# Kernel optimization log

Measured on AMD Instinct MI355X. Metric: run time of the kernel, lower is better.

## Reference

```python
import jax, jax.numpy as jnp
import numpy as np

N_ATOMS = 25000
N_PAIRS = 500000
N_PROP = 16
C = 64          # channel width of pp/pi/ii/out layers
N_BASIS = 4     # radial basis functions per pair
DEPTH = 4       # number of GC blocks


def setup_inputs() -> dict:
    key = jax.random.key(0)
    ks = jax.random.split(key, 16)

    def w(k, shape):
        fan_in = shape[-2]
        return jax.random.normal(k, shape, jnp.float32) / jnp.sqrt(jnp.float32(fan_in))

    return {
        "ind_2": jax.random.randint(ks[0], (N_PAIRS, 2), 0, N_ATOMS),
        "prop": jax.random.normal(ks[1], (N_ATOMS, N_PROP), jnp.float32),
        "basis": jax.random.uniform(ks[2], (N_PAIRS, N_BASIS), jnp.float32),
        "pp0_w1": w(ks[3], (N_PROP, C)),
        "pp0_b1": jnp.zeros((C,), jnp.float32),
        "pp_w1": w(ks[4], (DEPTH - 1, C, C)),
        "pp_b1": jnp.zeros((DEPTH - 1, C), jnp.float32),
        "pp_w2": w(ks[5], (DEPTH, C, C)),
        "pp_b2": jnp.zeros((DEPTH, C), jnp.float32),
        "pi_w1": w(ks[6], (DEPTH, 2 * C, C)),
        "pi_b1": jnp.zeros((DEPTH, C), jnp.float32),
        "pi_w2": w(ks[7], (DEPTH, C, C * N_BASIS)),
        "pi_b2": jnp.zeros((DEPTH, C * N_BASIS), jnp.float32),
        "ii_w1": w(ks[8], (DEPTH, C, C)),
        "ii_w2": w(ks[9], (DEPTH, C, C)),
        "res0_w": w(ks[10], (N_PROP, C)),
        "out_w1": w(ks[11], (DEPTH, C, C)),
        "out_b1": jnp.zeros((DEPTH, C), jnp.float32),
        "out_w2": w(ks[12], (DEPTH, C, C)),
        "out_b2": jnp.zeros((DEPTH, C), jnp.float32),
        "out_wo": w(ks[13], (DEPTH, C, 1)),
    }


def _pinet_forward(ind_2, prop, basis,
                   pp0_w1, pp0_b1, pp_w1, pp_b1, pp_w2, pp_b2,
                   pi_w1, pi_b1, pi_w2, pi_b2,
                   ii_w1, ii_w2, res0_w,
                   out_w1, out_b1, out_w2, out_b2, out_wo):
    act = jnp.tanh
    n_atoms = prop.shape[0]
    n_basis = basis.shape[-1]
    c = pi_w2.shape[-1] // n_basis  # pi output channels
    depth = pp_w2.shape[0]
    ind_i = ind_2[:, 0]
    ind_j = ind_2[:, 1]

    p = prop
    output = jnp.zeros((n_atoms, out_wo.shape[-1]), p.dtype)
    for d in range(depth):
        # PPLayer (FFLayer with bias)
        if d == 0:
            h = act(p @ pp0_w1 + pp0_b1)
        else:
            h = act(p @ pp_w1[d - 1] + pp_b1[d - 1])
        h = act(h @ pp_w2[d] + pp_b2[d])
        # PILayer: gather pair endpoints, concat, FFLayer, basis contraction
        pij = jnp.concatenate([h[ind_i], h[ind_j]], axis=-1)  # (P, 2C)
        ww = act(pij @ pi_w1[d] + pi_b1[d])                   # (P, C)
        ww = act(ww @ pi_w2[d] + pi_b2[d])                    # (P, C*B)
        ww = ww.reshape(-1, c, n_basis)                       # (P, C, B)
        inter = jnp.einsum('pcb,pb->pc', ww, basis)           # (P, C)
        # IILayer (FFLayer, no bias)
        inter = act(inter @ ii_w1[d])
        inter = act(inter @ ii_w2[d])
        # IPLayer: scatter-sum pairs back to atoms
        newp = jax.ops.segment_sum(inter, ind_i, num_segments=n_atoms)
        # ResUpdate: linear projection if dims differ (block 0), else plain sum
        p = (p @ res0_w + newp) if d == 0 else (p + newp)
        # OutLayer: FFLayer + biasless linear, accumulated over depth
        o = act(p @ out_w1[d] + out_b1[d])
        o = act(o @ out_w2[d] + out_b2[d])
        output = output + o @ out_wo[d]
    return output


def reference(ind_2, prop, basis,
              pp0_w1, pp0_b1, pp_w1, pp_b1, pp_w2, pp_b2,
              pi_w1, pi_b1, pi_w2, pi_b2,
              ii_w1, ii_w2, res0_w,
              out_w1, out_b1, out_w2, out_b2, out_wo):
    return _pinet_forward(ind_2, prop, basis,
                          pp0_w1, pp0_b1, pp_w1, pp_b1, pp_w2, pp_b2,
                          pi_w1, pi_b1, pi_w2, pi_b2,
                          ii_w1, ii_w2, res0_w,
                          out_w1, out_b1, out_w2, out_b2, out_wo)
```

## Files before the change

kernel.cpp:

```cpp
#include <hip/hip_runtime.h>
#include <hip/hip_bf16.h>

#define N_ATOMS 25000
#define N_PAIRS 500000
#define DEPTH 4

typedef _Float16 f16x8 __attribute__((ext_vector_type(8)));
typedef float f32x16 __attribute__((ext_vector_type(16)));
typedef unsigned short u16;

__device__ __forceinline__ float tanh_fast(float x) {
    float e = __expf(2.0f * x);
    return 1.0f - 2.0f * __builtin_amdgcn_rcpf(e + 1.0f);
}

__device__ __forceinline__ void split_h(float x, u16& hi, u16& lo) {
    _Float16 h = (_Float16)x;
    _Float16 l = (_Float16)(x - (float)h);
    hi = *(u16*)&h;
    lo = *(u16*)&l;
}

__device__ __forceinline__ void bar_lgkm() {
    asm volatile("s_waitcnt lgkmcnt(0)" ::: "memory");
    __builtin_amdgcn_s_barrier();
}

__device__ __forceinline__ int swz8(int u) { return u ^ ((u >> 5) & 7); }

__global__ __launch_bounds__(256)
void prep_kernel(const float* __restrict__ piW1, const float* __restrict__ piW2,
                 const float* __restrict__ iiW1, const float* __restrict__ iiW2,
                 u16* __restrict__ img1, u16* __restrict__ img2, u16* __restrict__ imgab) {
    int gid = blockIdx.x * 256 + threadIdx.x;
    int d = gid >> 15, e = gid & 32767;
    u16 hi, lo;
    if (e < 8192) {
        int k = e >> 6, n = e & 63;
        split_h(piW1[d * 8192 + e], hi, lo);
        int ntw = n >> 5, colb = n & 31;
        int ks = k >> 4, lh = (k >> 3) & 1, j = k & 7;
        int off = ((ntw * 8 + ks) * 64 + lh * 32 + colb) * 8 + j;
        img1[d * 16384 + 0 * 8192 + off] = hi;
        img1[d * 16384 + 1 * 8192 + off] = lo;
    } else if (e < 24576) {
        int s = e - 8192;
        int k = s >> 8, n = s & 255;
        split_h(piW2[d * 16384 + s], hi, lo);
        int ch = n >> 2, t = n & 3;
        int ntw = ch >> 5, colb = ch & 31;
        int ks = k >> 4, lh = (k >> 3) & 1, j = k & 7;
        int off = (((ntw * 4 + t) * 4 + ks) * 64 + lh * 32 + colb) * 8 + j;
        img2[d * 32768 + 0 * 16384 + off] = hi;
        img2[d * 32768 + 1 * 16384 + off] = lo;
    } else {
        int stage = (e < 28672) ? 0 : 1;
        int s = e - (stage ? 28672 : 24576);
        int k = s >> 6, n = s & 63;
        float x = stage ? iiW2[d * 4096 + s] : iiW1[d * 4096 + s];
        split_h(x, hi, lo);
        int ntw = n >> 5, colb = n & 31;
        int ks = k >> 4, lh = (k >> 3) & 1, j = k & 7;
        int off = ((ntw * 4 + ks) * 64 + lh * 32 + colb) * 8 + j;
        imgab[d * 16384 + (stage * 2 + 0) * 4096 + off] = hi;
        imgab[d * 16384 + (stage * 2 + 1) * 4096 + off] = lo;
    }
}

__global__ __launch_bounds__(256)
void prep_b2(const float* __restrict__ piB2, float* __restrict__ b2p) {
    int d = blockIdx.x, n = threadIdx.x;
    int ch = n >> 2, t = n & 3;
    int np = (ch >> 5) * 128 + t * 32 + (ch & 31);
    b2p[d * 256 + np] = piB2[d * 256 + n];
}

template <int K, bool IS_D0>
__global__ __launch_bounds__(256)
void atom_mlp(const float* __restrict__ p_in,
              const float* __restrict__ W1, const float* __restrict__ b1,
              const float* __restrict__ W2, const float* __restrict__ b2,
              const float* __restrict__ res0_w,
              _Float16* __restrict__ h_hi, _Float16* __restrict__ h_lo,
              float* __restrict__ acc_out) {
    __shared__ float sP[4][64];
    __shared__ float sH[4][64];
    int tid = threadIdx.x;
    int al = tid >> 6, c = tid & 63;
    int a = blockIdx.x * 4 + al;
    if (c < K) sP[al][c] = p_in[a * K + c];
    __syncthreads();
    float s = b1[c];
#pragma unroll
    for (int k = 0; k < K; ++k) s += sP[al][k] * W1[k * 64 + c];
    float t1 = tanh_fast(s);
    float r;
    if (IS_D0) {
        r = 0.f;
#pragma unroll
        for (int k = 0; k < 16; ++k) r += sP[al][k] * res0_w[k * 64 + c];
    } else {
        r = sP[al][c];
    }
    acc_out[a * 64 + c] = r;
    sH[al][c] = t1;
    __syncthreads();
    float s2 = b2[c];
#pragma unroll
    for (int k = 0; k < 64; ++k) s2 += sH[al][k] * W2[k * 64 + c];
    float hv = tanh_fast(s2);
    _Float16 hb = (_Float16)hv;
    h_hi[a * 64 + c] = hb;
    h_lo[a * 64 + c] = (_Float16)(hv - (float)hb);
}

__global__ __launch_bounds__(256)
void out_kernel(const float* __restrict__ p,
                const float* __restrict__ W1, const float* __restrict__ b1,
                const float* __restrict__ W2, const float* __restrict__ b2,
                const float* __restrict__ wo,
                float* __restrict__ out, int store) {
    __shared__ float sP[4][64];
    __shared__ float sH[4][64];
    int tid = threadIdx.x;
    int al = tid >> 6, c = tid & 63;
    int a = blockIdx.x * 4 + al;
    sP[al][c] = p[a * 64 + c];
    __syncthreads();
    float s = b1[c];
#pragma unroll
    for (int k = 0; k < 64; ++k) s += sP[al][k] * W1[k * 64 + c];
    sH[al][c] = tanh_fast(s);
    __syncthreads();
    float s2 = b2[c];
#pragma unroll
    for (int k = 0; k < 64; ++k) s2 += sH[al][k] * W2[k * 64 + c];
    float v = tanh_fast(s2) * wo[c];
#pragma unroll
    for (int off = 32; off > 0; off >>= 1) v += __shfl_down(v, off, 64);
    if (c == 0) {
        if (store) out[a] = v;
        else out[a] += v;
    }
}

__global__ __launch_bounds__(256)
void fused_out_atom(const float* __restrict__ p,
                    const float* __restrict__ oW1, const float* __restrict__ ob1,
                    const float* __restrict__ oW2, const float* __restrict__ ob2,
                    const float* __restrict__ wo,
                    const float* __restrict__ aW1, const float* __restrict__ ab1,
                    const float* __restrict__ aW2, const float* __restrict__ ab2,
                    float* __restrict__ out, int store,
                    _Float16* __restrict__ h_hi, _Float16* __restrict__ h_lo,
                    float* __restrict__ acc_out) {
    __shared__ float sP[4][64];
    __shared__ float sHo[4][64];
    __shared__ float sHa[4][64];
    int tid = threadIdx.x;
    int al = tid >> 6, c = tid & 63;
    int a = blockIdx.x * 4 + al;
    float pv = p[a * 64 + c];
    sP[al][c] = pv;
    acc_out[a * 64 + c] = pv;
    __syncthreads();
    float so = ob1[c], sa = ab1[c];
#pragma unroll
    for (int k = 0; k < 64; ++k) {
        float x = sP[al][k];
        so += x * oW1[k * 64 + c];
        sa += x * aW1[k * 64 + c];
    }
    sHo[al][c] = tanh_fast(so);
    sHa[al][c] = tanh_fast(sa);
    __syncthreads();
    float s2o = ob2[c], s2a = ab2[c];
#pragma unroll
    for (int k = 0; k < 64; ++k) {
        s2o += sHo[al][k] * oW2[k * 64 + c];
        s2a += sHa[al][k] * aW2[k * 64 + c];
    }
    float v = tanh_fast(s2o) * wo[c];
#pragma unroll
    for (int off = 32; off > 0; off >>= 1) v += __shfl_down(v, off, 64);
    if (c == 0) {
        if (store) out[a] = v;
        else out[a] += v;
    }
    float hv = tanh_fast(s2a);
    _Float16 hb = (_Float16)hv;
    h_hi[a * 64 + c] = hb;
    h_lo[a * 64 + c] = (_Float16)(hv - (float)hb);
}

#define MFMA __builtin_amdgcn_mfma_f32_32x32x16_f16

__global__ __launch_bounds__(512, 2)
void pair_kernel(const _Float16* __restrict__ hhi,
                 const _Float16* __restrict__ hlo,
                 const int* __restrict__ ind2,
                 const float* __restrict__ basis,
                 const u16* __restrict__ img1,
                 const u16* __restrict__ img2,
                 const u16* __restrict__ imgab,
                 const float* __restrict__ piB1,
                 const float* __restrict__ b2p,
                 float* __restrict__ accp) {
    __shared__ __attribute__((aligned(16))) _Float16 sW2[32768];
    __shared__ __attribute__((aligned(16))) _Float16 sW1lo[8192];
    __shared__ __attribute__((aligned(16))) _Float16 sA[16384];
    __shared__ __attribute__((aligned(16))) _Float16 sAlo[8192];
    __shared__ __attribute__((aligned(16))) _Float16 sPing[8192];
    __shared__ float sBas[2][128 * 4];
    __shared__ int sIdx[2][128];

    const int tid = threadIdx.x;
    for (int i = tid; i < 4096; i += 512) ((uint4*)sW2)[i] = ((const uint4*)img2)[i];
    for (int i = tid; i < 1024; i += 512) ((uint4*)sW1lo)[i] = ((const uint4*)(img1 + 8192))[i];

    const int l = tid & 63;
    const int w = tid >> 6;
    const int mt = w >> 1, ntw = w & 1;
    const int col = l & 31, kg = l >> 5;
    const int ch = ntw * 32 + col;
    const int chks = ch >> 4, chlh = (ch >> 3) & 1, chj = ch & 7;

    int rb[4], wb[4];
    {
        const int wxor = 2 * chks + chlh;
#pragma unroll
        for (int c = 0; c < 4; ++c) {
            rb[c] = (l ^ (kg + 2 * c)) << 4;
            wb[c] = (mt * 4 + chks) * 1024 + chlh * 512 + ((((c) + 4 * kg) ^ wxor) << 4) + chj * 2;
        }
    }
    const int mtsA = mt << 13;
    const int mts  = mt << 12;

    f16x8 w1h[8], fa[2][4], fb[2][4];
#pragma unroll
    for (int ks = 0; ks < 8; ++ks)
        w1h[ks] = *(const f16x8*)(img1 + ntw * 4096 + ks * 512 + l * 8);
#pragma unroll
    for (int hl = 0; hl < 2; ++hl)
#pragma unroll
        for (int ks = 0; ks < 4; ++ks) {
            fa[hl][ks] = *(const f16x8*)(imgab + (0 * 2 + hl) * 4096 + ntw * 2048 + ks * 512 + l * 8);
            fb[hl][ks] = *(const f16x8*)(imgab + (1 * 2 + hl) * 4096 + ntw * 2048 + ks * 512 + l * 8);
        }
    const float b1v = piB1[ch];
    float b2v[4];
#pragma unroll
    for (int t = 0; t < 4; ++t) b2v[t] = b2p[ntw * 128 + t * 32 + col];

    const int nTiles = (N_PAIRS + 127) >> 7;

    auto gather = [&](int tile, int pb) {
        int base = tile << 7;
        if (tid < 128) {
            int p = base + tid;
            float4 bv = (p < N_PAIRS) ? ((const float4*)basis)[p] : make_float4(0.f, 0.f, 0.f, 0.f);
            *(float4*)&sBas[pb][tid * 4] = bv;
            sIdx[pb][tid] = (p < N_PAIRS) ? ind2[2 * p] : 0;
        }
#pragma unroll
        for (int it = 0; it < 6; ++it) {
            int id = it * 512 + tid;
            if (id < 2048) {
                int m = id >> 4, half = (id >> 3) & 1, seg = id & 7;
                int p = base + m;
                uint4 v = make_uint4(0u, 0u, 0u, 0u);
                if (p < N_PAIRS) {
                    int row = ind2[2 * p + half];
                    v = *(const uint4*)(hhi + row * 64 + seg * 8);
                }
                int mtd = m >> 5, lrow = m & 31;
                int ks = half * 4 + (seg >> 1), lh = seg & 1;
                int u = (mtd * 8 + ks) * 64 + lh * 32 + lrow;
                *(uint4*)(sA + swz8(u) * 8) = v;
            } else {
                int e = id - 2048;
                int m = e >> 3, seg = e & 7;
                int p = base + m;
                uint4 v = make_uint4(0u, 0u, 0u, 0u);
                if (p < N_PAIRS) {
                    int row = ind2[2 * p];
                    v = *(const uint4*)(hlo + row * 64 + seg * 8);
                }
                int mtd = m >> 5, lrow = m & 31;
                int ks = seg >> 1, lh = seg & 1;
                int u = (mtd * 4 + ks) * 64 + lh * 32 + lrow;
                *(uint4*)(sAlo + swz8(u) * 8) = v;
            }
        }
    };
    gather(blockIdx.x, 0);
    __syncthreads();

    int pb = 0;
    for (int tile = blockIdx.x; tile < nTiles; tile += gridDim.x) {
        const int base = tile << 7;

        {
            f32x16 acc = {};
            const char* blo = (const char*)(sW1lo + ntw * 4096 + l * 8);
#pragma unroll
            for (int ks = 0; ks < 8; ++ks) {
                f16x8 a = *(const f16x8*)((const char*)sA + mtsA + ks * 1024 + rb[ks & 3]);
                acc = MFMA(a, w1h[ks], acc, 0, 0, 0);
                acc = MFMA(a, *(const f16x8*)(blo + ks * 1024), acc, 0, 0, 0);
            }
#pragma unroll
            for (int ks = 0; ks < 4; ++ks) {
                f16x8 a = *(const f16x8*)((const char*)sAlo + mts + ks * 1024 + rb[ks]);
                acc = MFMA(a, w1h[ks], acc, 0, 0, 0);
            }
#pragma unroll
            for (int r = 0; r < 16; ++r)
                *(u16*)((char*)sPing + wb[r & 3] + ((r >> 2) << 7)) =
                    __builtin_bit_cast(u16, (_Float16)tanh_fast(acc[r] + b1v));
        }
        bar_lgkm();

        {
            f32x16 acc[4] = {{}, {}, {}, {}};
#pragma unroll
            for (int ks = 0; ks < 4; ++ks) {
                f16x8 a = *(const f16x8*)((const char*)sPing + mts + ks * 1024 + rb[ks]);
#pragma unroll
                for (int t = 0; t < 4; ++t) {
                    acc[t] = MFMA(a, *(const f16x8*)(sW2 + ((ntw * 4 + t) * 4 + ks) * 512 + l * 8), acc[t], 0, 0, 0);
                    acc[t] = MFMA(a, *(const f16x8*)(sW2 + 16384 + ((ntw * 4 + t) * 4 + ks) * 512 + l * 8), acc[t], 0, 0, 0);
                }
            }
#pragma unroll
            for (int r = 0; r < 16; ++r) {
                int lrow = (r & 3) + 8 * (r >> 2) + 4 * kg;
                int row = mt * 32 + lrow;
                float4 bas = *(const float4*)&sBas[pb][row * 4];
                float s = tanh_fast(acc[0][r] + b2v[0]) * bas.x
                        + tanh_fast(acc[1][r] + b2v[1]) * bas.y
                        + tanh_fast(acc[2][r] + b2v[2]) * bas.z
                        + tanh_fast(acc[3][r] + b2v[3]) * bas.w;
                *(u16*)((char*)sA + wb[r & 3] + ((r >> 2) << 7)) =
                    __builtin_bit_cast(u16, (_Float16)s);
            }
        }
        bar_lgkm();

        {
            f32x16 acc = {};
#pragma unroll
            for (int ks = 0; ks < 4; ++ks) {
                f16x8 a = *(const f16x8*)((const char*)sA + mts + ks * 1024 + rb[ks]);
                acc = MFMA(a, fa[0][ks], acc, 0, 0, 0);
                acc = MFMA(a, fa[1][ks], acc, 0, 0, 0);
            }
#pragma unroll
            for (int r = 0; r < 16; ++r)
                *(u16*)((char*)sPing + wb[r & 3] + ((r >> 2) << 7)) =
                    __builtin_bit_cast(u16, (_Float16)tanh_fast(acc[r]));
        }
        bar_lgkm();

        {
            f16x8 afr[4];
#pragma unroll
            for (int ks = 0; ks < 4; ++ks)
                afr[ks] = *(const f16x8*)((const char*)sPing + mts + ks * 1024 + rb[ks]);

            gather(tile + gridDim.x, pb ^ 1);

            f32x16 acc = {};
#pragma unroll
            for (int ks = 0; ks < 4; ++ks) {
                acc = MFMA(afr[ks], fb[0][ks], acc, 0, 0, 0);
                acc = MFMA(afr[ks], fb[1][ks], acc, 0, 0, 0);
            }
#pragma unroll
            for (int r = 0; r < 16; ++r) {
                int lrow = (r & 3) + 8 * (r >> 2) + 4 * kg;
                int p = base + mt * 32 + lrow;
                if (p < N_PAIRS)
                    atomicAdd(&accp[sIdx[pb][mt * 32 + lrow] * 64 + ch], tanh_fast(acc[r]));
            }
        }
        bar_lgkm();
        pb ^= 1;
    }
}

extern "C" void kernel_launch(void* const* d_in, const int* in_sizes, int n_in,
                              void* d_out, int out_size, void* d_ws, size_t ws_size,
                              hipStream_t stream) {
    const int* ind2 = (const int*)d_in[0];
    const float* prop = (const float*)d_in[1];
    const float* basis = (const float*)d_in[2];
    const float* pp0_w1 = (const float*)d_in[3];
    const float* pp0_b1 = (const float*)d_in[4];
    const float* pp_w1 = (const float*)d_in[5];
    const float* pp_b1 = (const float*)d_in[6];
    const float* pp_w2 = (const float*)d_in[7];
    const float* pp_b2 = (const float*)d_in[8];
    const float* pi_w1 = (const float*)d_in[9];
    const float* pi_b1 = (const float*)d_in[10];
    const float* pi_w2 = (const float*)d_in[11];
    const float* pi_b2 = (const float*)d_in[12];
    const float* ii_w1 = (const float*)d_in[13];
    const float* ii_w2 = (const float*)d_in[14];
    const float* res0_w = (const float*)d_in[15];
    const float* out_w1 = (const float*)d_in[16];
    const float* out_b1 = (const float*)d_in[17];
    const float* out_w2 = (const float*)d_in[18];
    const float* out_b2 = (const float*)d_in[19];
    const float* out_wo = (const float*)d_in[20];
    float* out = (float*)d_out;

    float* B0 = (float*)d_ws;
    float* B1 = B0 + N_ATOMS * 64;
    _Float16* Hhi = (_Float16*)(B1 + N_ATOMS * 64);
    _Float16* Hlo = Hhi + N_ATOMS * 64;
    u16* img1 = (u16*)(Hlo + N_ATOMS * 64);
    u16* img2 = img1 + 4 * 16384;
    u16* imgab = img2 + 4 * 32768;
    float* b2p = (float*)(imgab + 4 * 16384);
    float* pbuf[2] = {B0, B1};

    prep_kernel<<<512, 256, 0, stream>>>(pi_w1, pi_w2, ii_w1, ii_w2, img1, img2, imgab);
    prep_b2<<<4, 256, 0, stream>>>(pi_b2, b2p);

    for (int d = 0; d < DEPTH; ++d) {
        float* acc = pbuf[d & 1];
        if (d == 0) {
            atom_mlp<16, true><<<N_ATOMS / 4, 256, 0, stream>>>(
                prop, pp0_w1, pp0_b1, pp_w2, pp_b2, res0_w, Hhi, Hlo, acc);
        } else {
            const float* pin = pbuf[(d - 1) & 1];
            fused_out_atom<<<N_ATOMS / 4, 256, 0, stream>>>(
                pin,
                out_w1 + (d - 1) * 4096, out_b1 + (d - 1) * 64,
                out_w2 + (d - 1) * 4096, out_b2 + (d - 1) * 64, out_wo + (d - 1) * 64,
                pp_w1 + (d - 1) * 4096, pp_b1 + (d - 1) * 64,
                pp_w2 + d * 4096, pp_b2 + d * 64,
                out, (d - 1) == 0 ? 1 : 0,
                Hhi, Hlo, acc);
        }
        pair_kernel<<<256, 512, 0, stream>>>(
            Hhi, Hlo, ind2, basis,
            img1 + d * 16384, img2 + d * 32768, imgab + d * 16384,
            pi_b1 + d * 64, b2p + d * 256, acc);
    }
    out_kernel<<<N_ATOMS / 4, 256, 0, stream>>>(
        pbuf[(DEPTH - 1) & 1], out_w1 + (DEPTH - 1) * 4096, out_b1 + (DEPTH - 1) * 64,
        out_w2 + (DEPTH - 1) * 4096, out_b2 + (DEPTH - 1) * 64, out_wo + (DEPTH - 1) * 64,
        out, 0);
}
```

Before: 1.043 ms.

## Precompute per-atom pi first-layer projections and gather them in the pair kernel

The first pi layer is linear in the concatenated pair features, so it is split into per-atom projections U = h·W1[:64] and V = h·W1[64:], computed once per atom in the atom MLP kernels. The pair kernel then gathers fp32 U/V rows, adds them with the bias and applies tanh, which removes the per-pair W1 MFMA stage and the hi/lo fp16 split of h. The pair kernel also moves to 192-pair tiles with 768 threads, reads the ii weights from LDS instead of registers, and processes the basis contraction in two passes to save registers. In exchange it gathers twice as many bytes per pair (fp32 instead of fp16), drops the double-buffered gather of the next tile, and adds atom-side matmul work.

```diff
diff --git a/kernel.cpp b/kernel.cpp
--- a/kernel.cpp
+++ b/kernel.cpp
@@ -4,6 +4,8 @@
 #define N_ATOMS 25000
 #define N_PAIRS 500000
 #define DEPTH 4
+#define TILE 192
+#define PTHREADS 768
 
 typedef _Float16 f16x8 __attribute__((ext_vector_type(8)));
 typedef float f32x16 __attribute__((ext_vector_type(16)));
@@ -19,11 +21,6 @@
     _Float16 l = (_Float16)(x - (float)h);
     hi = *(u16*)&h;
     lo = *(u16*)&l;
-}
-
-__device__ __forceinline__ void bar_lgkm() {
-    asm volatile("s_waitcnt lgkmcnt(0)" ::: "memory");
-    __builtin_amdgcn_s_barrier();
 }
 
 __device__ __forceinline__ int swz8(int u) { return u ^ ((u >> 5) & 7); }
@@ -81,10 +78,12 @@
               const float* __restrict__ W1, const float* __restrict__ b1,
               const float* __restrict__ W2, const float* __restrict__ b2,
               const float* __restrict__ res0_w,
-              _Float16* __restrict__ h_hi, _Float16* __restrict__ h_lo,
+              const float* __restrict__ piW1d,
+              float* __restrict__ Uo, float* __restrict__ Vo,
               float* __restrict__ acc_out) {
     __shared__ float sP[4][64];
     __shared__ float sH[4][64];
+    __shared__ float sH2[4][64];
     int tid = threadIdx.x;
     int al = tid >> 6, c = tid & 63;
     int a = blockIdx.x * 4 + al;
@@ -109,9 +108,17 @@
 #pragma unroll
     for (int k = 0; k < 64; ++k) s2 += sH[al][k] * W2[k * 64 + c];
     float hv = tanh_fast(s2);
-    _Float16 hb = (_Float16)hv;
-    h_hi[a * 64 + c] = hb;
-    h_lo[a * 64 + c] = (_Float16)(hv - (float)hb);
+    sH2[al][c] = hv;
+    __syncthreads();
+    float su = 0.f, sv = 0.f;
+#pragma unroll
+    for (int k = 0; k < 64; ++k) {
+        float x = sH2[al][k];
+        su += x * piW1d[k * 64 + c];
+        sv += x * piW1d[(64 + k) * 64 + c];
+    }
+    Uo[a * 64 + c] = su;
+    Vo[a * 64 + c] = sv;
 }
 
 __global__ __launch_bounds__(256)
@@ -152,7 +159,8 @@
                     const float* __restrict__ aW1, const float* __restrict__ ab1,
                     const float* __restrict__ aW2, const float* __restrict__ ab2,
                     float* __restrict__ out, int store,
-                    _Float16* __restrict__ h_hi, _Float16* __restrict__ h_lo,
+                    const float* __restrict__ piW1d,
+                    float* __restrict__ Uo, float* __restrict__ Vo,
                     float* __restrict__ acc_out) {
     __shared__ float sP[4][64];
     __shared__ float sHo[4][64];
@@ -188,35 +196,41 @@
         else out[a] += v;
     }
     float hv = tanh_fast(s2a);
-    _Float16 hb = (_Float16)hv;
-    h_hi[a * 64 + c] = hb;
-    h_lo[a * 64 + c] = (_Float16)(hv - (float)hb);
+    sP[al][c] = hv;
+    __syncthreads();
+    float su = 0.f, sv = 0.f;
+#pragma unroll
+    for (int k = 0; k < 64; ++k) {
+        float x = sP[al][k];
+        su += x * piW1d[k * 64 + c];
+        sv += x * piW1d[(64 + k) * 64 + c];
+    }
+    Uo[a * 64 + c] = su;
+    Vo[a * 64 + c] = sv;
 }
 
 #define MFMA __builtin_amdgcn_mfma_f32_32x32x16_f16
 
-__global__ __launch_bounds__(512, 2)
-void pair_kernel(const _Float16* __restrict__ hhi,
-                 const _Float16* __restrict__ hlo,
+__global__ __launch_bounds__(PTHREADS, 3)
+void pair_kernel(const float* __restrict__ Uin,
+                 const float* __restrict__ Vin,
                  const int* __restrict__ ind2,
                  const float* __restrict__ basis,
-                 const u16* __restrict__ img1,
                  const u16* __restrict__ img2,
                  const u16* __restrict__ imgab,
                  const float* __restrict__ piB1,
                  const float* __restrict__ b2p,
                  float* __restrict__ accp) {
     __shared__ __attribute__((aligned(16))) _Float16 sW2[32768];
-    __shared__ __attribute__((aligned(16))) _Float16 sW1lo[8192];
-    __shared__ __attribute__((aligned(16))) _Float16 sA[16384];
-    __shared__ __attribute__((aligned(16))) _Float16 sAlo[8192];
-    __shared__ __attribute__((aligned(16))) _Float16 sPing[8192];
-    __shared__ float sBas[2][128 * 4];
-    __shared__ int sIdx[2][128];
+    __shared__ __attribute__((aligned(16))) u16 sAB[16384];
+    __shared__ __attribute__((aligned(16))) _Float16 bufA[12288];
+    __shared__ __attribute__((aligned(16))) _Float16 bufB[12288];
+    __shared__ float sBas[TILE * 4];
+    __shared__ int sIdx[TILE];
 
     const int tid = threadIdx.x;
-    for (int i = tid; i < 4096; i += 512) ((uint4*)sW2)[i] = ((const uint4*)img2)[i];
-    for (int i = tid; i < 1024; i += 512) ((uint4*)sW1lo)[i] = ((const uint4*)(img1 + 8192))[i];
+    for (int i = tid; i < 4096; i += PTHREADS) ((uint4*)sW2)[i] = ((const uint4*)img2)[i];
+    for (int i = tid; i < 2048; i += PTHREADS) ((uint4*)sAB)[i] = ((const uint4*)imgab)[i];
 
     const int l = tid & 63;
     const int w = tid >> 6;
@@ -234,159 +248,134 @@
             wb[c] = (mt * 4 + chks) * 1024 + chlh * 512 + ((((c) + 4 * kg) ^ wxor) << 4) + chj * 2;
         }
     }
-    const int mtsA = mt << 13;
-    const int mts  = mt << 12;
-
-    f16x8 w1h[8], fa[2][4], fb[2][4];
-#pragma unroll
-    for (int ks = 0; ks < 8; ++ks)
-        w1h[ks] = *(const f16x8*)(img1 + ntw * 4096 + ks * 512 + l * 8);
-#pragma unroll
-    for (int hl = 0; hl < 2; ++hl)
-#pragma unroll
-        for (int ks = 0; ks < 4; ++ks) {
-            fa[hl][ks] = *(const f16x8*)(imgab + (0 * 2 + hl) * 4096 + ntw * 2048 + ks * 512 + l * 8);
-            fb[hl][ks] = *(const f16x8*)(imgab + (1 * 2 + hl) * 4096 + ntw * 2048 + ks * 512 + l * 8);
-        }
-    const float b1v = piB1[ch];
+    const int mts = mt << 12;
+
+    const int m = tid >> 2, ksel = tid & 3;
+    const int mtd = m >> 5, lrow = m & 31;
+    const int u0 = (mtd * 4 + ksel) * 64 + lrow;
+    const int wA0 = swz8(u0) * 16, wA1 = swz8(u0 + 32) * 16;
+
+    float b1p[16];
+#pragma unroll
+    for (int z = 0; z < 16; ++z) b1p[z] = piB1[ksel * 16 + z];
     float b2v[4];
 #pragma unroll
     for (int t = 0; t < 4; ++t) b2v[t] = b2p[ntw * 128 + t * 32 + col];
 
-    const int nTiles = (N_PAIRS + 127) >> 7;
-
-    auto gather = [&](int tile, int pb) {
-        int base = tile << 7;
-        if (tid < 128) {
+    const int nTiles = (N_PAIRS + TILE - 1) / TILE;
+
+    float ur[16], vr[16];
+    auto loadUV = [&](int tile) {
+        int p = tile * TILE + m;
+        bool ok = (tile < nTiles) && (p < N_PAIRS);
+        int2 ij = ok ? ((const int2*)ind2)[p] : make_int2(0, 0);
+        const float* up = Uin + ij.x * 64 + ksel * 16;
+        const float* vp = Vin + ij.y * 64 + ksel * 16;
+        float4 z4 = make_float4(0.f, 0.f, 0.f, 0.f);
+#pragma unroll
+        for (int q = 0; q < 4; ++q) {
+            float4 a = ok ? *(const float4*)(up + q * 4) : z4;
+            float4 b = ok ? *(const float4*)(vp + q * 4) : z4;
+            ur[q * 4 + 0] = a.x; ur[q * 4 + 1] = a.y; ur[q * 4 + 2] = a.z; ur[q * 4 + 3] = a.w;
+            vr[q * 4 + 0] = b.x; vr[q * 4 + 1] = b.y; vr[q * 4 + 2] = b.z; vr[q * 4 + 3] = b.w;
+        }
+    };
+    loadUV(blockIdx.x);
+
+    for (int tile = blockIdx.x; tile < nTiles; tile += gridDim.x) {
+        const int base = tile * TILE;
+
+        if (tid < TILE) {
             int p = base + tid;
             float4 bv = (p < N_PAIRS) ? ((const float4*)basis)[p] : make_float4(0.f, 0.f, 0.f, 0.f);
-            *(float4*)&sBas[pb][tid * 4] = bv;
-            sIdx[pb][tid] = (p < N_PAIRS) ? ind2[2 * p] : 0;
-        }
-#pragma unroll
-        for (int it = 0; it < 6; ++it) {
-            int id = it * 512 + tid;
-            if (id < 2048) {
-                int m = id >> 4, half = (id >> 3) & 1, seg = id & 7;
-                int p = base + m;
-                uint4 v = make_uint4(0u, 0u, 0u, 0u);
-                if (p < N_PAIRS) {
-                    int row = ind2[2 * p + half];
-                    v = *(const uint4*)(hhi + row * 64 + seg * 8);
+            *(float4*)&sBas[tid * 4] = bv;
+            sIdx[tid] = (p < N_PAIRS) ? ind2[2 * p] : 0;
+        }
+        {
+            f16x8 lo8, hi8;
+#pragma unroll
+            for (int z = 0; z < 8; ++z)
+                lo8[z] = (_Float16)tanh_fast(ur[z] + vr[z] + b1p[z]);
+#pragma unroll
+            for (int z = 0; z < 8; ++z)
+                hi8[z] = (_Float16)tanh_fast(ur[8 + z] + vr[8 + z] + b1p[8 + z]);
+            *(f16x8*)((char*)bufA + wA0) = lo8;
+            *(f16x8*)((char*)bufA + wA1) = hi8;
+        }
+        __syncthreads();
+
+        {
+            f16x8 afr[4];
+#pragma unroll
+            for (int ks = 0; ks < 4; ++ks)
+                afr[ks] = *(const f16x8*)((const char*)bufA + mts + ks * 1024 + rb[ks]);
+            float s[16];
+#pragma unroll
+            for (int r = 0; r < 16; ++r) s[r] = 0.f;
+#pragma unroll
+            for (int pp = 0; pp < 2; ++pp) {
+                f32x16 a0 = {}, a1 = {};
+                const int t0 = 2 * pp, t1 = 2 * pp + 1;
+#pragma unroll
+                for (int ks = 0; ks < 4; ++ks) {
+                    a0 = MFMA(afr[ks], *(const f16x8*)(sW2 + ((ntw * 4 + t0) * 4 + ks) * 512 + l * 8), a0, 0, 0, 0);
+                    a0 = MFMA(afr[ks], *(const f16x8*)(sW2 + 16384 + ((ntw * 4 + t0) * 4 + ks) * 512 + l * 8), a0, 0, 0, 0);
+                    a1 = MFMA(afr[ks], *(const f16x8*)(sW2 + ((ntw * 4 + t1) * 4 + ks) * 512 + l * 8), a1, 0, 0, 0);
+                    a1 = MFMA(afr[ks], *(const f16x8*)(sW2 + 16384 + ((ntw * 4 + t1) * 4 + ks) * 512 + l * 8), a1, 0, 0, 0);
                 }
-                int mtd = m >> 5, lrow = m & 31;
-                int ks = half * 4 + (seg >> 1), lh = seg & 1;
-                int u = (mtd * 8 + ks) * 64 + lh * 32 + lrow;
-                *(uint4*)(sA + swz8(u) * 8) = v;
-            } else {
-                int e = id - 2048;
-                int m = e >> 3, seg = e & 7;
-                int p = base + m;
-                uint4 v = make_uint4(0u, 0u, 0u, 0u);
-                if (p < N_PAIRS) {
-                    int row = ind2[2 * p];
-                    v = *(const uint4*)(hlo + row * 64 + seg * 8);
-                }
-                int mtd = m >> 5, lrow = m & 31;
-                int ks = seg >> 1, lh = seg & 1;
-                int u = (mtd * 4 + ks) * 64 + lh * 32 + lrow;
-                *(uint4*)(sAlo + swz8(u) * 8) = v;
-            }
-        }
-    };
-    gather(blockIdx.x, 0);
-    __syncthreads();
-
-    int pb = 0;
-    for (int tile = blockIdx.x; tile < nTiles; tile += gridDim.x) {
-        const int base = tile << 7;
-
-        {
-            f32x16 acc = {};
-            const char* blo = (const char*)(sW1lo + ntw * 4096 + l * 8);
-#pragma unroll
-            for (int ks = 0; ks < 8; ++ks) {
-                f16x8 a = *(const f16x8*)((const char*)sA + mtsA + ks * 1024 + rb[ks & 3]);
-                acc = MFMA(a, w1h[ks], acc, 0, 0, 0);
-                acc = MFMA(a, *(const f16x8*)(blo + ks * 1024), acc, 0, 0, 0);
-            }
-#pragma unroll
-            for (int ks = 0; ks < 4; ++ks) {
-                f16x8 a = *(const f16x8*)((const char*)sAlo + mts + ks * 1024 + rb[ks]);
-                acc = MFMA(a, w1h[ks], acc, 0, 0, 0);
-            }
-#pragma unroll
-            for (int r = 0; r < 16; ++r)
-                *(u16*)((char*)sPing + wb[r & 3] + ((r >> 2) << 7)) =
-                    __builtin_bit_cast(u16, (_Float16)tanh_fast(acc[r] + b1v));
-        }
-        bar_lgkm();
-
-        {
-            f32x16 acc[4] = {{}, {}, {}, {}};
-#pragma unroll
-            for (int ks = 0; ks < 4; ++ks) {
-                f16x8 a = *(const f16x8*)((const char*)sPing + mts + ks * 1024 + rb[ks]);
-#pragma unroll
-                for (int t = 0; t < 4; ++t) {
-                    acc[t] = MFMA(a, *(const f16x8*)(sW2 + ((ntw * 4 + t) * 4 + ks) * 512 + l * 8), acc[t], 0, 0, 0);
-                    acc[t] = MFMA(a, *(const f16x8*)(sW2 + 16384 + ((ntw * 4 + t) * 4 + ks) * 512 + l * 8), acc[t], 0, 0, 0);
+#pragma unroll
+                for (int r = 0; r < 16; ++r) {
+                    int lr2 = (r & 3) + 8 * (r >> 2) + 4 * kg;
+                    int row = mt * 32 + lr2;
+                    float2 bb = *(const float2*)&sBas[row * 4 + 2 * pp];
+                    s[r] += tanh_fast(a0[r] + b2v[t0]) * bb.x + tanh_fast(a1[r] + b2v[t1]) * bb.y;
                 }
             }
 #pragma unroll
-            for (int r = 0; r < 16; ++r) {
-                int lrow = (r & 3) + 8 * (r >> 2) + 4 * kg;
-                int row = mt * 32 + lrow;
-                float4 bas = *(const float4*)&sBas[pb][row * 4];
-                float s = tanh_fast(acc[0][r] + b2v[0]) * bas.x
-                        + tanh_fast(acc[1][r] + b2v[1]) * bas.y
-                        + tanh_fast(acc[2][r] + b2v[2]) * bas.z
-                        + tanh_fast(acc[3][r] + b2v[3]) * bas.w;
-                *(u16*)((char*)sA + wb[r & 3] + ((r >> 2) << 7)) =
-                    __builtin_bit_cast(u16, (_Float16)s);
+            for (int r = 0; r < 16; ++r)
+                *(u16*)((char*)bufB + wb[r & 3] + ((r >> 2) << 7)) =
+                    __builtin_bit_cast(u16, (_Float16)s[r]);
+        }
+        __syncthreads();
+
+        {
+            f32x16 ah = {}, al2 = {};
+#pragma unroll
+            for (int ks = 0; ks < 4; ++ks) {
+                f16x8 a = *(const f16x8*)((const char*)bufB + mts + ks * 1024 + rb[ks]);
+                ah  = MFMA(a, *(const f16x8*)(sAB + 0 * 4096 + ntw * 2048 + ks * 512 + l * 8), ah, 0, 0, 0);
+                al2 = MFMA(a, *(const f16x8*)(sAB + 1 * 4096 + ntw * 2048 + ks * 512 + l * 8), al2, 0, 0, 0);
             }
-        }
-        bar_lgkm();
-
-        {
-            f32x16 acc = {};
-#pragma unroll
-            for (int ks = 0; ks < 4; ++ks) {
-                f16x8 a = *(const f16x8*)((const char*)sA + mts + ks * 1024 + rb[ks]);
-                acc = MFMA(a, fa[0][ks], acc, 0, 0, 0);
-                acc = MFMA(a, fa[1][ks], acc, 0, 0, 0);
-            }
 #pragma unroll
             for (int r = 0; r < 16; ++r)
-                *(u16*)((char*)sPing + wb[r & 3] + ((r >> 2) << 7)) =
-                    __builtin_bit_cast(u16, (_Float16)tanh_fast(acc[r]));
-        }
-        bar_lgkm();
+                *(u16*)((char*)bufA + wb[r & 3] + ((r >> 2) << 7)) =
+                    __builtin_bit_cast(u16, (_Float16)tanh_fast(ah[r] + al2[r]));
+        }
+        __syncthreads();
 
         {
             f16x8 afr[4];
 #pragma unroll
             for (int ks = 0; ks < 4; ++ks)
-                afr[ks] = *(const f16x8*)((const char*)sPing + mts + ks * 1024 + rb[ks]);
-
-            gather(tile + gridDim.x, pb ^ 1);
-
-            f32x16 acc = {};
+                afr[ks] = *(const f16x8*)((const char*)bufA + mts + ks * 1024 + rb[ks]);
+
+            loadUV(tile + gridDim.x);
+
+            f32x16 ah = {}, al2 = {};
 #pragma unroll
             for (int ks = 0; ks < 4; ++ks) {
-                acc = MFMA(afr[ks], fb[0][ks], acc, 0, 0, 0);
-                acc = MFMA(afr[ks], fb[1][ks], acc, 0, 0, 0);
+                ah  = MFMA(afr[ks], *(const f16x8*)(sAB + 2 * 4096 + ntw * 2048 + ks * 512 + l * 8), ah, 0, 0, 0);
+                al2 = MFMA(afr[ks], *(const f16x8*)(sAB + 3 * 4096 + ntw * 2048 + ks * 512 + l * 8), al2, 0, 0, 0);
             }
 #pragma unroll
             for (int r = 0; r < 16; ++r) {
-                int lrow = (r & 3) + 8 * (r >> 2) + 4 * kg;
-                int p = base + mt * 32 + lrow;
+                int lr2 = (r & 3) + 8 * (r >> 2) + 4 * kg;
+                int p = base + mt * 32 + lr2;
                 if (p < N_PAIRS)
-                    atomicAdd(&accp[sIdx[pb][mt * 32 + lrow] * 64 + ch], tanh_fast(acc[r]));
+                    atomicAdd(&accp[sIdx[mt * 32 + lr2] * 64 + ch], tanh_fast(ah[r] + al2[r]));
             }
         }
-        bar_lgkm();
-        pb ^= 1;
+        __syncthreads();
     }
 }
 
@@ -418,9 +407,9 @@
 
     float* B0 = (float*)d_ws;
     float* B1 = B0 + N_ATOMS * 64;
-    _Float16* Hhi = (_Float16*)(B1 + N_ATOMS * 64);
-    _Float16* Hlo = Hhi + N_ATOMS * 64;
-    u16* img1 = (u16*)(Hlo + N_ATOMS * 64);
+    float* Ubuf = B1 + N_ATOMS * 64;
+    float* Vbuf = Ubuf + N_ATOMS * 64;
+    u16* img1 = (u16*)(Vbuf + N_ATOMS * 64);
     u16* img2 = img1 + 4 * 16384;
     u16* imgab = img2 + 4 * 32768;
     float* b2p = (float*)(imgab + 4 * 16384);
@@ -433,7 +422,8 @@
         float* acc = pbuf[d & 1];
         if (d == 0) {
             atom_mlp<16, true><<<N_ATOMS / 4, 256, 0, stream>>>(
-                prop, pp0_w1, pp0_b1, pp_w2, pp_b2, res0_w, Hhi, Hlo, acc);
+                prop, pp0_w1, pp0_b1, pp_w2, pp_b2, res0_w,
+                pi_w1, Ubuf, Vbuf, acc);
         } else {
             const float* pin = pbuf[(d - 1) & 1];
             fused_out_atom<<<N_ATOMS / 4, 256, 0, stream>>>(
@@ -443,11 +433,11 @@
                 pp_w1 + (d - 1) * 4096, pp_b1 + (d - 1) * 64,
                 pp_w2 + d * 4096, pp_b2 + d * 64,
                 out, (d - 1) == 0 ? 1 : 0,
-                Hhi, Hlo, acc);
-        }
-        pair_kernel<<<256, 512, 0, stream>>>(
-            Hhi, Hlo, ind2, basis,
-            img1 + d * 16384, img2 + d * 32768, imgab + d * 16384,
+                pi_w1 + d * 8192, Ubuf, Vbuf, acc);
+        }
+        pair_kernel<<<256, PTHREADS, 0, stream>>>(
+            Ubuf, Vbuf, ind2, basis,
+            img2 + d * 32768, imgab + d * 16384,
             pi_b1 + d * 64, b2p + d * 256, acc);
     }
     out_kernel<<<N_ATOMS / 4, 256, 0, stream>>>(
```

Result: slower. 1.368 ms (+31.2%).
